# Kernel tuning notes

Hardware: AMD Instinct MI355X
Metric: run time of the kernel (lower is better)

## Reference

```python
import jax, jax.numpy as jnp
import numpy as np

N_LAYER = 4
N_EMBD = 768
N_HEAD = 12
B, T = 4, 1024  # T = 4 * t, t = 256 (block_size)
EPS = 1e-5


def layernorm(x, g, b):
    mu = jnp.mean(x, axis=-1, keepdims=True)
    var = jnp.var(x, axis=-1, keepdims=True)
    return (x - mu) * jax.lax.rsqrt(var + EPS) * g + b


def setup_inputs() -> dict:
    key = jax.random.key(0)
    ks = jax.random.split(key, 20)
    C, L, H = N_EMBD, N_LAYER, 4 * N_EMBD
    std = 0.02
    inp = {
        "x": jax.random.normal(ks[0], (B, T, C), dtype=jnp.float32),
        "ln1_g": jnp.ones((L, C), jnp.float32),
        "ln1_b": jnp.zeros((L, C), jnp.float32),
        "Wq": std * jax.random.normal(ks[1], (L, C, C), jnp.float32),
        "bq": jnp.zeros((L, C), jnp.float32),
        "Wk": std * jax.random.normal(ks[2], (L, C, C), jnp.float32),
        "bk": jnp.zeros((L, C), jnp.float32),
        "Wv": std * jax.random.normal(ks[3], (L, C, C), jnp.float32),
        "bv": jnp.zeros((L, C), jnp.float32),
        "Wp": std * jax.random.normal(ks[4], (L, C, C), jnp.float32),
        "bp": jnp.zeros((L, C), jnp.float32),
        "ln2_g": jnp.ones((L, C), jnp.float32),
        "ln2_b": jnp.zeros((L, C), jnp.float32),
        "W1": std * jax.random.normal(ks[5], (L, C, H), jnp.float32),
        "b1": jnp.zeros((L, H), jnp.float32),
        "W2": std * jax.random.normal(ks[6], (L, H, C), jnp.float32),
        "b2": jnp.zeros((L, C), jnp.float32),
    }
    return inp


def _forward(x, ln1_g, ln1_b, Wq, bq, Wk, bk, Wv, bv, Wp, bp, ln2_g, ln2_b, W1, b1, W2, b2):
    Bx, Tx, C = x.shape
    hd = C // N_HEAD
    t = Tx // 4
    # cross-conditional mask: causal tril(t,t) tiled 4x4 over the 4 streams
    mask = jnp.tile(jnp.tril(jnp.ones((t, t), dtype=bool)), (4, 4))  # [T, T]
    scale = 1.0 / np.sqrt(hd).astype(np.float32)

    def block(h, p):
        (g1, b1g, wq, bqv, wk, bkv, wv, bvv, wp, bpv, g2, b2g, w1, b1v, w2, b2v) = p
        a_in = layernorm(h, g1, b1g)
        q = (a_in @ wq + bqv).reshape(Bx, Tx, N_HEAD, hd).transpose(0, 2, 1, 3)
        k = (a_in @ wk + bkv).reshape(Bx, Tx, N_HEAD, hd).transpose(0, 2, 1, 3)
        v = (a_in @ wv + bvv).reshape(Bx, Tx, N_HEAD, hd).transpose(0, 2, 1, 3)
        att = jnp.einsum('bhqd,bhkd->bhqk', q, k) * scale
        att = jnp.where(mask, att, -jnp.inf)
        att = jax.nn.softmax(att, axis=-1)
        y = jnp.einsum('bhqk,bhkd->bhqd', att, v)
        y = y.transpose(0, 2, 1, 3).reshape(Bx, Tx, C)
        h = h + (y @ wp + bpv)
        m_in = layernorm(h, g2, b2g)
        m = jax.nn.gelu(m_in @ w1 + b1v, approximate=False) @ w2 + b2v
        return h + m, None

    params = (ln1_g, ln1_b, Wq, bq, Wk, bk, Wv, bv, Wp, bp, ln2_g, ln2_b, W1, b1, W2, b2)
    x, _ = jax.lax.scan(block, x, params)
    return x


def reference(x, ln1_g, ln1_b, Wq, bq, Wk, bk, Wv, bv, Wp, bp, ln2_g, ln2_b, W1, b1, W2, b2):
    return _forward(x, ln1_g, ln1_b, Wq, bq, Wk, bk, Wv, bv, Wp, bp, ln2_g, ln2_b, W1, b1, W2, b2)
```

## Files before the change

### kernel.cpp

```cpp
#include <hip/hip_runtime.h>
#include <hip/hip_bf16.h>
#include <math.h>

typedef __hip_bfloat16 bf16;
typedef __attribute__((ext_vector_type(8))) short bf16x8;
typedef __attribute__((ext_vector_type(4))) float f32x4;

#define CDIM 768
#define HDIM 64
#define NHEAD 12
#define TSEQ 1024
#define MROWS 4096
#define HID 3072
#define QKVN 2304

__device__ inline void gld16(const void* g, void* l) {
  __builtin_amdgcn_global_load_lds((const __attribute__((address_space(1))) void*)g,
                                   (__attribute__((address_space(3))) void*)l, 16, 0, 0);
}

__global__ void k_transall(const float* __restrict__ Wq, const float* __restrict__ Wk,
                           const float* __restrict__ Wv, const float* __restrict__ Wp,
                           const float* __restrict__ W1, const float* __restrict__ W2,
                           const float* __restrict__ bq, const float* __restrict__ bk,
                           const float* __restrict__ bv,
                           bf16* __restrict__ wqkv, bf16* __restrict__ wtp,
                           bf16* __restrict__ wt1, bf16* __restrict__ wt2,
                           float* __restrict__ bqkv) {
  __shared__ float t[32][33];
  int blk = blockIdx.x;
  if (blk >= 6912) {
    int i = (blk - 6912) * 256 + threadIdx.y * 32 + threadIdx.x;
    if (i < QKVN) bqkv[i] = (i < CDIM) ? bq[i] : (i < 2 * CDIM) ? bk[i - CDIM] : bv[i - 2 * CDIM];
    return;
  }
  const float* src; bf16* dst; int K, N, n0, k0;
  if (blk < 1728) {
    int w = blk / 576, id = blk % 576;
    src = (w == 0) ? Wq : (w == 1) ? Wk : Wv;
    dst = wqkv + (size_t)w * CDIM * CDIM;
    K = CDIM; N = CDIM;
    n0 = (id % 24) * 32; k0 = (id / 24) * 32;
  } else if (blk < 2304) {
    int id = blk - 1728;
    src = Wp; dst = wtp; K = CDIM; N = CDIM;
    n0 = (id % 24) * 32; k0 = (id / 24) * 32;
  } else if (blk < 4608) {
    int id = blk - 2304;
    src = W1; dst = wt1; K = CDIM; N = HID;
    n0 = (id % 96) * 32; k0 = (id / 96) * 32;
  } else {
    int id = blk - 4608;
    src = W2; dst = wt2; K = HID; N = CDIM;
    n0 = (id % 24) * 32; k0 = (id / 24) * 32;
  }
  int c = threadIdx.x, ry = threadIdx.y;
  #pragma unroll
  for (int i = 0; i < 4; i++) {
    int r = ry + 8 * i;
    t[r][c] = src[(size_t)(k0 + r) * N + n0 + c];
  }
  __syncthreads();
  #pragma unroll
  for (int i = 0; i < 4; i++) {
    int r = ry + 8 * i;
    dst[(size_t)(n0 + r) * K + k0 + c] = __float2bfloat16(t[c][r]);
  }
}

__global__ __launch_bounds__(256) void k_ln(const float* __restrict__ h, const float* __restrict__ g,
                                            const float* __restrict__ b, bf16* __restrict__ out) {
  int row = blockIdx.x, tid = threadIdx.x;
  const float* hr = h + (size_t)row * CDIM;
  float x0 = hr[tid], x1 = hr[tid + 256], x2 = hr[tid + 512];
  float s = x0 + x1 + x2;
  float ss = x0 * x0 + x1 * x1 + x2 * x2;
  #pragma unroll
  for (int off = 32; off > 0; off >>= 1) {
    s  += __shfl_down(s, off, 64);
    ss += __shfl_down(ss, off, 64);
  }
  __shared__ float rs[4], rq[4];
  if ((tid & 63) == 0) { rs[tid >> 6] = s; rq[tid >> 6] = ss; }
  __syncthreads();
  s  = rs[0] + rs[1] + rs[2] + rs[3];
  ss = rq[0] + rq[1] + rq[2] + rq[3];
  float mu = s * (1.0f / CDIM);
  float var = ss * (1.0f / CDIM) - mu * mu;
  float rstd = rsqrtf(var + 1e-5f);
  bf16* orow = out + (size_t)row * CDIM;
  orow[tid]       = __float2bfloat16((x0 - mu) * rstd * g[tid]       + b[tid]);
  orow[tid + 256] = __float2bfloat16((x1 - mu) * rstd * g[tid + 256] + b[tid + 256]);
  orow[tid + 512] = __float2bfloat16((x2 - mu) * rstd * g[tid + 512] + b[tid + 512]);
}


template <int BM, int BN, int EPI>
__global__ __launch_bounds__(256) void k_gemmT(const bf16* __restrict__ A, const bf16* __restrict__ Bt,
                                               const float* __restrict__ bias,
                                               void* __restrict__ outv, int M, int N, int K) {
  constexpr int MR = BM / 32, NR = BN / 32;
  __shared__ __align__(16) bf16 As[BM * 64];
  __shared__ __align__(16) bf16 Bs[BN * 64];
  int tid = threadIdx.x;
  int m0 = blockIdx.x * BM, n0 = blockIdx.y * BN;
  int wave = tid >> 6, lane = tid & 63;
  int wr = wave >> 1, wc = wave & 1;
  int lrow = lane & 15, quad = lane >> 4;
  int sw = lrow & 7;
  f32x4 zz = {0.f, 0.f, 0.f, 0.f};
  f32x4 acc[MR][NR];
  #pragma unroll
  for (int i = 0; i < MR; i++)
    #pragma unroll
    for (int j = 0; j < NR; j++) acc[i][j] = zz;
  const bf16* Ag = A + (size_t)m0 * K;
  const bf16* Bg = Bt + (size_t)n0 * K;
  for (int k0 = 0; k0 < K; k0 += 64) {
    __syncthreads();
    #pragma unroll
    for (int i = 0; i < BM / 32; i++) {
      int idx = i * 256 + tid;
      int row = idx >> 3, c = idx & 7;
      gld16(Ag + (size_t)row * K + k0 + ((c ^ (row & 7)) * 8), As + idx * 8);
    }
    #pragma unroll
    for (int i = 0; i < BN / 32; i++) {
      int idx = i * 256 + tid;
      int row = idx >> 3, c = idx & 7;
      gld16(Bg + (size_t)row * K + k0 + ((c ^ (row & 7)) * 8), Bs + idx * 8);
    }
    __syncthreads();
    #pragma unroll
    for (int kc = 0; kc < 2; kc++) {
      int g = kc * 4 + quad;
      bf16x8 af[MR], bfr[NR];
      #pragma unroll
      for (int mi = 0; mi < MR; mi++)
        af[mi] = *(const bf16x8*)(As + (wr * (BM / 2) + mi * 16 + lrow) * 64 + ((g ^ sw) * 8));
      #pragma unroll
      for (int ni = 0; ni < NR; ni++)
        bfr[ni] = *(const bf16x8*)(Bs + (wc * (BN / 2) + ni * 16 + lrow) * 64 + ((g ^ sw) * 8));
      #pragma unroll
      for (int mi = 0; mi < MR; mi++)
        #pragma unroll
        for (int ni = 0; ni < NR; ni++)
          acc[mi][ni] = __builtin_amdgcn_mfma_f32_16x16x32_bf16(af[mi], bfr[ni], acc[mi][ni], 0, 0, 0);
    }
  }
  #pragma unroll
  for (int ni = 0; ni < NR; ni++) {
    int gc = n0 + wc * (BN / 2) + ni * 16 + lrow;
    float bval = bias[gc];
    #pragma unroll
    for (int mi = 0; mi < MR; mi++) {
      #pragma unroll
      for (int r = 0; r < 4; r++) {
        int grow = m0 + wr * (BM / 2) + mi * 16 + quad * 4 + r;
        float vv = acc[mi][ni][r] + bval;
        if (EPI == 1) vv = 0.5f * vv * (1.0f + erff(vv * 0.70710678118654752f));
        if (EPI == 2) {
          float* hp = (float*)outv + (size_t)grow * N + gc;
          *hp = *hp + vv;
        } else {
          ((bf16*)outv)[(size_t)grow * N + gc] = __float2bfloat16(vv);
        }
      }
    }
  }
}

__global__ __launch_bounds__(256) void k_attn(const bf16* __restrict__ qkv, bf16* __restrict__ y) {
  int bh = blockIdx.x;
  int b = bh / NHEAD, hh = bh % NHEAD;
  int qc = blockIdx.y;
  int tid = threadIdx.x;
  int wave = tid >> 6, lane = tid & 63;
  int lrow = lane & 15, quad = lane >> 4;
  int sw = lrow & 7;
  int q0 = qc * 64 + wave * 16;
  int qmod = q0 & 255;
  int qcmod = (qc * 64) & 255;

  const size_t rstride = QKVN;
  const bf16* qbase = qkv + (size_t)(b * TSEQ) * rstride + hh * HDIM;
  const bf16* kbase = qbase + CDIM;
  const bf16* vbase = qbase + 2 * CDIM;

  bf16x8 qf[2];
  #pragma unroll
  for (int kc = 0; kc < 2; kc++)
    qf[kc] = *(const bf16x8*)(qbase + (size_t)(q0 + lrow) * rstride + kc * 32 + quad * 8);

  f32x4 zz = {0.f, 0.f, 0.f, 0.f};
  f32x4 Oacc[4];
  #pragma unroll
  for (int j = 0; j < 4; j++) Oacc[j] = zz;
  float m[4] = {-1e30f, -1e30f, -1e30f, -1e30f};
  float l[4] = {0.f, 0.f, 0.f, 0.f};

  __shared__ __align__(16) bf16 Ks[64 * 64];
  __shared__ __align__(16) bf16 Vt[64 * 72];
  __shared__ __align__(16) bf16 Pl[4][16 * 64];

  for (int kt = 0; kt < 16; kt++) {
    int k0 = kt * 64;
    int kmod = k0 & 255;
    if (kmod > qcmod + 63) continue;
    __syncthreads();
    #pragma unroll
    for (int i = 0; i < 2; i++) {
      int idx = i * 256 + tid;
      int key = idx >> 3, c = idx & 7;
      gld16(kbase + (size_t)(k0 + key) * rstride + ((c ^ (key & 7)) * 8), Ks + idx * 8);
      int vkey = idx & 63, vd0 = (idx >> 6) * 8;
      bf16x8 vv = *(const bf16x8*)(vbase + (size_t)(k0 + vkey) * rstride + vd0);
      const bf16* vp = (const bf16*)&vv;
      #pragma unroll
      for (int j = 0; j < 8; j++) Vt[(vd0 + j) * 72 + vkey] = vp[j];
    }
    __syncthreads();
    if (kmod > qmod + 15) continue;

    f32x4 s[4];
    #pragma unroll
    for (int sub = 0; sub < 4; sub++) {
      s[sub] = zz;
      #pragma unroll
      for (int kc = 0; kc < 2; kc++) {
        int g = kc * 4 + quad;
        bf16x8 kf = *(const bf16x8*)(Ks + (sub * 16 + lrow) * 64 + ((g ^ sw) * 8));
        s[sub] = __builtin_amdgcn_mfma_f32_16x16x32_bf16(qf[kc], kf, s[sub], 0, 0, 0);
      }
    }
    bool partial = (kmod + 63 > qmod);
    #pragma unroll
    for (int sub = 0; sub < 4; sub++)
      #pragma unroll
      for (int r = 0; r < 4; r++) {
        float sv = s[sub][r] * 0.125f;
        if (partial) {
          int krel = kmod + sub * 16 + lrow;
          int qrel = qmod + quad * 4 + r;
          if (krel > qrel) sv = -1e30f;
        }
        s[sub][r] = sv;
      }
    float pr[4][4], alpha[4];
    #pragma unroll
    for (int r = 0; r < 4; r++) {
      float v = fmaxf(fmaxf(s[0][r], s[1][r]), fmaxf(s[2][r], s[3][r]));
      v = fmaxf(v, __shfl_xor(v, 1, 64));
      v = fmaxf(v, __shfl_xor(v, 2, 64));
      v = fmaxf(v, __shfl_xor(v, 4, 64));
      v = fmaxf(v, __shfl_xor(v, 8, 64));
      float mnew = fmaxf(m[r], v);
      alpha[r] = __expf(m[r] - mnew);
      m[r] = mnew;
      float rsum = 0.f;
      #pragma unroll
      for (int sub = 0; sub < 4; sub++) {
        pr[sub][r] = __expf(s[sub][r] - mnew);
        rsum += pr[sub][r];
      }
      rsum += __shfl_xor(rsum, 1, 64);
      rsum += __shfl_xor(rsum, 2, 64);
      rsum += __shfl_xor(rsum, 4, 64);
      rsum += __shfl_xor(rsum, 8, 64);
      l[r] = l[r] * alpha[r] + rsum;
    }
    #pragma unroll
    for (int j = 0; j < 4; j++)
      #pragma unroll
      for (int r = 0; r < 4; r++) Oacc[j][r] *= alpha[r];
    bf16* Pw = (bf16*)Pl[wave];
    #pragma unroll
    for (int sub = 0; sub < 4; sub++) {
      int cc = sub * 2 + (lrow >> 3);
      int e = lrow & 7;
      #pragma unroll
      for (int r = 0; r < 4; r++) {
        int mm = quad * 4 + r;
        Pw[mm * 64 + ((cc ^ (mm & 7)) * 8) + e] = __float2bfloat16(pr[sub][r]);
      }
    }
    bf16x8 pf[2];
    #pragma unroll
    for (int kc = 0; kc < 2; kc++) {
      int g = kc * 4 + quad;
      pf[kc] = *(const bf16x8*)(Pw + lrow * 64 + ((g ^ sw) * 8));
    }
    #pragma unroll
    for (int j = 0; j < 4; j++)
      #pragma unroll
      for (int kc = 0; kc < 2; kc++) {
        bf16x8 vf = *(const bf16x8*)(Vt + (j * 16 + lrow) * 72 + kc * 32 + quad * 8);
        Oacc[j] = __builtin_amdgcn_mfma_f32_16x16x32_bf16(pf[kc], vf, Oacc[j], 0, 0, 0);
      }
  }
  #pragma unroll
  for (int r = 0; r < 4; r++) {
    float inv = 1.0f / l[r];
    bf16* yp = y + (size_t)(b * TSEQ + q0 + quad * 4 + r) * CDIM + hh * HDIM;
    #pragma unroll
    for (int j = 0; j < 4; j++)
      yp[j * 16 + lrow] = __float2bfloat16(Oacc[j][r] * inv);
  }
}

extern "C" void kernel_launch(void* const* d_in, const int* in_sizes, int n_in,
                              void* d_out, int out_size, void* d_ws, size_t ws_size,
                              hipStream_t stream) {
  const float* x    = (const float*)d_in[0];
  const float* ln1g = (const float*)d_in[1];
  const float* ln1b = (const float*)d_in[2];
  const float* Wq   = (const float*)d_in[3];
  const float* bq   = (const float*)d_in[4];
  const float* Wk   = (const float*)d_in[5];
  const float* bk   = (const float*)d_in[6];
  const float* Wv   = (const float*)d_in[7];
  const float* bv   = (const float*)d_in[8];
  const float* Wp   = (const float*)d_in[9];
  const float* bp   = (const float*)d_in[10];
  const float* ln2g = (const float*)d_in[11];
  const float* ln2b = (const float*)d_in[12];
  const float* W1   = (const float*)d_in[13];
  const float* b1   = (const float*)d_in[14];
  const float* W2   = (const float*)d_in[15];
  const float* b2   = (const float*)d_in[16];

  char* ws = (char*)d_ws;
  size_t off = 0;
  float* h    = (float*)(ws + off); off += (size_t)MROWS * CDIM * 4;
  bf16* a     = (bf16*)(ws + off);  off += (size_t)MROWS * CDIM * 2;
  bf16* qkvb  = (bf16*)(ws + off);  off += (size_t)MROWS * QKVN * 2;
  bf16* yb    = (bf16*)(ws + off);  off += (size_t)MROWS * CDIM * 2;
  bf16* m1    = qkvb;
  bf16* wqkv  = (bf16*)(ws + off);  off += (size_t)QKVN * CDIM * 2;
  bf16* wtp   = (bf16*)(ws + off);  off += (size_t)CDIM * CDIM * 2;
  bf16* wt1   = (bf16*)(ws + off);  off += (size_t)CDIM * HID * 2;
  bf16* wt2   = (bf16*)(ws + off);  off += (size_t)CDIM * HID * 2;
  float* bqkv = (float*)(ws + off); off += (size_t)QKVN * 4;

  int n = MROWS * CDIM;
  hipMemcpyAsync(h, x, (size_t)n * sizeof(float), hipMemcpyDeviceToDevice, stream);

  for (int l = 0; l < 4; l++) {
    const float* Wql = Wq + (size_t)l * CDIM * CDIM;
    const float* Wkl = Wk + (size_t)l * CDIM * CDIM;
    const float* Wvl = Wv + (size_t)l * CDIM * CDIM;
    const float* Wpl = Wp + (size_t)l * CDIM * CDIM;
    const float* W1l = W1 + (size_t)l * CDIM * HID;
    const float* W2l = W2 + (size_t)l * HID * CDIM;

    k_transall<<<dim3(6921), dim3(32, 8), 0, stream>>>(Wql, Wkl, Wvl, Wpl, W1l, W2l,
                                                       bq + l * CDIM, bk + l * CDIM, bv + l * CDIM,
                                                       wqkv, wtp, wt1, wt2, bqkv);

    k_ln<<<dim3(MROWS), dim3(256), 0, stream>>>(h, ln1g + l * CDIM, ln1b + l * CDIM, a);

    k_gemmT<128, 128, 0><<<dim3(MROWS / 128, QKVN / 128), dim3(256), 0, stream>>>(
        a, wqkv, bqkv, qkvb, MROWS, QKVN, CDIM);

    k_attn<<<dim3(4 * NHEAD, 16), dim3(256), 0, stream>>>(qkvb, yb);

    k_gemmT<64, 64, 2><<<dim3(MROWS / 64, CDIM / 64), dim3(256), 0, stream>>>(
        yb, wtp, bp + (size_t)l * CDIM, h, MROWS, CDIM, CDIM);

    k_ln<<<dim3(MROWS), dim3(256), 0, stream>>>(h, ln2g + l * CDIM, ln2b + l * CDIM, a);

    k_gemmT<128, 128, 1><<<dim3(MROWS / 128, HID / 128), dim3(256), 0, stream>>>(
        a, wt1, b1 + (size_t)l * HID, m1, MROWS, HID, CDIM);

    k_gemmT<64, 64, 2><<<dim3(MROWS / 64, CDIM / 64), dim3(256), 0, stream>>>(
        m1, wt2, b2 + (size_t)l * CDIM, h, MROWS, CDIM, HID);
  }

  hipMemcpyAsync(d_out, h, (size_t)n * sizeof(float), hipMemcpyDeviceToDevice, stream);
}
```

Baseline: 928.2 us.

## Double-buffer LDS tiles in GEMM to overlap global loads with MFMA

Splits the GEMM shared-memory tiles into two buffers and prefetches the next K-tile via global_load_lds while computing on the current one. This is meant to hide global memory latency that was previously exposed by the load-sync-compute sequence, and it halves the number of barriers per tile pair. It doubles LDS usage, which can lower occupancy. It also assumes the K-tile count is even; K=768 and K=3072 satisfy that.

Result: slower. 949.1 us (+2.2%).

```diff
diff --git a/kernel.cpp b/kernel.cpp
--- a/kernel.cpp
+++ b/kernel.cpp
@@ -100,8 +100,8 @@
                                                const float* __restrict__ bias,
                                                void* __restrict__ outv, int M, int N, int K) {
   constexpr int MR = BM / 32, NR = BN / 32;
-  __shared__ __align__(16) bf16 As[BM * 64];
-  __shared__ __align__(16) bf16 Bs[BN * 64];
+  __shared__ __align__(16) bf16 As[2][BM * 64];
+  __shared__ __align__(16) bf16 Bs[2][BN * 64];
   int tid = threadIdx.x;
   int m0 = blockIdx.x * BM, n0 = blockIdx.y * BN;
   int wave = tid >> 6, lane = tid & 63;
@@ -116,38 +116,60 @@
     for (int j = 0; j < NR; j++) acc[i][j] = zz;
   const bf16* Ag = A + (size_t)m0 * K;
   const bf16* Bg = Bt + (size_t)n0 * K;
-  for (int k0 = 0; k0 < K; k0 += 64) {
+
+#define STAGE(buf, kk)                                                                   \
+  {                                                                                      \
+    _Pragma("unroll")                                                                    \
+    for (int i = 0; i < BM / 32; i++) {                                                  \
+      int idx = i * 256 + tid;                                                           \
+      int row = idx >> 3, c = idx & 7;                                                   \
+      gld16(Ag + (size_t)row * K + (kk) + ((c ^ (row & 7)) * 8), As[buf] + idx * 8);     \
+    }                                                                                    \
+    _Pragma("unroll")                                                                    \
+    for (int i = 0; i < BN / 32; i++) {                                                  \
+      int idx = i * 256 + tid;                                                           \
+      int row = idx >> 3, c = idx & 7;                                                   \
+      gld16(Bg + (size_t)row * K + (kk) + ((c ^ (row & 7)) * 8), Bs[buf] + idx * 8);     \
+    }                                                                                    \
+  }
+
+#define COMPUTE(buf)                                                                     \
+  {                                                                                      \
+    _Pragma("unroll")                                                                    \
+    for (int kc = 0; kc < 2; kc++) {                                                     \
+      int g = kc * 4 + quad;                                                             \
+      bf16x8 af[MR], bfr[NR];                                                            \
+      _Pragma("unroll")                                                                  \
+      for (int mi = 0; mi < MR; mi++)                                                    \
+        af[mi] = *(const bf16x8*)(As[buf] + (wr * (BM / 2) + mi * 16 + lrow) * 64 +      \
+                                  ((g ^ sw) * 8));                                       \
+      _Pragma("unroll")                                                                  \
+      for (int ni = 0; ni < NR; ni++)                                                    \
+        bfr[ni] = *(const bf16x8*)(Bs[buf] + (wc * (BN / 2) + ni * 16 + lrow) * 64 +     \
+                                   ((g ^ sw) * 8));                                      \
+      _Pragma("unroll")                                                                  \
+      for (int mi = 0; mi < MR; mi++)                                                    \
+        _Pragma("unroll")                                                                \
+        for (int ni = 0; ni < NR; ni++)                                                  \
+          acc[mi][ni] =                                                                  \
+              __builtin_amdgcn_mfma_f32_16x16x32_bf16(af[mi], bfr[ni], acc[mi][ni], 0, 0, 0); \
+    }                                                                                    \
+  }
+
+  int nk = K >> 6;
+  STAGE(0, 0);
+  __syncthreads();
+  for (int t = 0; t < nk; t += 2) {
+    STAGE(1, (t + 1) << 6);
+    COMPUTE(0);
     __syncthreads();
-    #pragma unroll
-    for (int i = 0; i < BM / 32; i++) {
-      int idx = i * 256 + tid;
-      int row = idx >> 3, c = idx & 7;
-      gld16(Ag + (size_t)row * K + k0 + ((c ^ (row & 7)) * 8), As + idx * 8);
-    }
-    #pragma unroll
-    for (int i = 0; i < BN / 32; i++) {
-      int idx = i * 256 + tid;
-      int row = idx >> 3, c = idx & 7;
-      gld16(Bg + (size_t)row * K + k0 + ((c ^ (row & 7)) * 8), Bs + idx * 8);
-    }
+    if (t + 2 < nk) STAGE(0, (t + 2) << 6);
+    COMPUTE(1);
     __syncthreads();
-    #pragma unroll
-    for (int kc = 0; kc < 2; kc++) {
-      int g = kc * 4 + quad;
-      bf16x8 af[MR], bfr[NR];
-      #pragma unroll
-      for (int mi = 0; mi < MR; mi++)
-        af[mi] = *(const bf16x8*)(As + (wr * (BM / 2) + mi * 16 + lrow) * 64 + ((g ^ sw) * 8));
-      #pragma unroll
-      for (int ni = 0; ni < NR; ni++)
-        bfr[ni] = *(const bf16x8*)(Bs + (wc * (BN / 2) + ni * 16 + lrow) * 64 + ((g ^ sw) * 8));
-      #pragma unroll
-      for (int mi = 0; mi < MR; mi++)
-        #pragma unroll
-        for (int ni = 0; ni < NR; ni++)
-          acc[mi][ni] = __builtin_amdgcn_mfma_f32_16x16x32_bf16(af[mi], bfr[ni], acc[mi][ni], 0, 0, 0);
-    }
-  }
+  }
+#undef STAGE
+#undef COMPUTE
+
   #pragma unroll
   for (int ni = 0; ni < NR; ni++) {
     int gc = n0 + wc * (BN / 2) + ni * 16 + lrow;
```
